# Optimization experiments

Measured on AMD Instinct MI355X. Metric: run time of the kernel, lower is better.

The kernel has to match this reference:

```python
import jax, jax.numpy as jnp
import numpy as np

CLS_COST, BBOX_COST, GIOU_COST = 2.0, 5.0, 2.0


def box_cxcywh_to_xyxy(b):
    cx, cy, w, h = b[..., 0], b[..., 1], b[..., 2], b[..., 3]
    return jnp.stack([cx - 0.5 * w, cy - 0.5 * h, cx + 0.5 * w, cy + 0.5 * h], axis=-1)


def generalized_box_iou(a, b):
    # a: [B,Q,4] xyxy, b: [B,T,4] xyxy -> [B,Q,T]
    area_a = (a[..., 2] - a[..., 0]) * (a[..., 3] - a[..., 1])  # [B,Q]
    area_b = (b[..., 2] - b[..., 0]) * (b[..., 3] - b[..., 1])  # [B,T]
    lt = jnp.maximum(a[:, :, None, :2], b[:, None, :, :2])      # [B,Q,T,2]
    rb = jnp.minimum(a[:, :, None, 2:], b[:, None, :, 2:])
    wh = jnp.clip(rb - lt, 0.0)
    inter = wh[..., 0] * wh[..., 1]                              # [B,Q,T]
    union = area_a[:, :, None] + area_b[:, None, :] - inter
    iou = inter / union
    lt_c = jnp.minimum(a[:, :, None, :2], b[:, None, :, :2])
    rb_c = jnp.maximum(a[:, :, None, 2:], b[:, None, :, 2:])
    wh_c = jnp.clip(rb_c - lt_c, 0.0)
    area_c = wh_c[..., 0] * wh_c[..., 1]
    return iou - (area_c - union) / area_c


def setup_inputs() -> dict:
    key = jax.random.key(0)
    k1, k2, k3, k4 = jax.random.split(key, 4)
    B, Q, C, T = 256, 900, 80, 300
    pred_logits = jax.random.normal(k1, (B, Q, C), dtype=jnp.float32)
    pred_boxes = jax.random.uniform(k2, (B, Q, 4), dtype=jnp.float32)
    tgt_labels = jax.random.randint(k3, (B, T), 0, C)
    tgt_boxes = jax.random.uniform(k4, (B, T, 4), dtype=jnp.float32)
    return {"pred_logits": pred_logits, "pred_boxes": pred_boxes,
            "tgt_labels": tgt_labels, "tgt_boxes": tgt_boxes}


def reference(pred_logits, pred_boxes, tgt_labels, tgt_boxes):
    # cost_class[b,q,t] = -sigmoid(logits)[b,q,labels[b,t]]
    prob = jax.nn.sigmoid(pred_logits)                              # [B,Q,C]
    cost_class = -jnp.take_along_axis(prob, tgt_labels[:, None, :], axis=2)  # [B,Q,T]
    # L1 cdist in cxcywh space
    cost_bbox = jnp.abs(pred_boxes[:, :, None, :] - tgt_boxes[:, None, :, :]).sum(-1)
    cost_giou = -generalized_box_iou(box_cxcywh_to_xyxy(pred_boxes),
                                     box_cxcywh_to_xyxy(tgt_boxes))
    return CLS_COST * cost_class + BBOX_COST * cost_bbox + GIOU_COST * cost_giou
```

## Files before the change

### kernel.cpp

```cpp
#include <hip/hip_runtime.h>

#define QDIM 900
#define CDIM 80
#define TDIM 300
#define QPB 36
#define QPW 9
#define NQB (QDIM / QPB)

typedef float floatx4 __attribute__((ext_vector_type(4)));

struct TgtReg {
    float x0, y0, x1, y1;
    float cx, cy, w, h;
    float area;
    int   lab;
};

__device__ __forceinline__ float cost_one(
    float ax0, float ay0, float ax1, float ay1,
    float acx, float acy, float aw, float ah, float area_a,
    const float* __restrict__ clsrow, const TgtReg& t)
{
    float clsv = clsrow[t.lab];

    float M0x = fmaxf(ax0, t.x0);
    float m1x = fminf(ax1, t.x1);
    float iwr = m1x - M0x;
    float iw  = fmaxf(iwr, 0.0f);
    float cw  = (aw + t.w) - iwr;

    float M0y = fmaxf(ay0, t.y0);
    float m1y = fminf(ay1, t.y1);
    float ihr = m1y - M0y;
    float ih  = fmaxf(ihr, 0.0f);
    float ch  = (ah + t.h) - ihr;

    float inter = iw * ih;
    float areac = cw * ch;
    float uni   = (area_a + t.area) - inter;

    float num   = fmaf(uni, uni, inter * areac);
    float den   = uni * areac;
    float ratio = num * __builtin_amdgcn_rcpf(den);

    float l1 = fabsf(acx - t.cx) + fabsf(acy - t.cy)
             + fabsf(aw - t.w)   + fabsf(ah - t.h);

    float acc = fmaf(5.0f, l1, clsv);
    return fmaf(-2.0f, ratio, acc);
}

__device__ __forceinline__ TgtReg load_tgt(const float4* tb4, const int* lb, int t)
{
    TgtReg r;
    float4 v = tb4[t];
    r.cx = v.x; r.cy = v.y; r.w = v.z; r.h = v.w;
    float hw = 0.5f * v.z, hh = 0.5f * v.w;
    r.x0 = v.x - hw; r.y0 = v.y - hh;
    r.x1 = v.x + hw; r.y1 = v.y + hh;
    r.area = v.z * v.w;
    r.lab = lb[t];
    return r;
}

__global__ __launch_bounds__(256, 4) void matcher_cost_kernel(
    const float* __restrict__ pred_logits,
    const float* __restrict__ pred_boxes,
    const int*   __restrict__ tgt_labels,
    const float* __restrict__ tgt_boxes,
    float* __restrict__ out)
{
    __shared__ float s_cls[QPB * CDIM];

    const int tid = threadIdx.x;
    const int b  = blockIdx.x / NQB;
    const int q0 = (blockIdx.x % NQB) * QPB;

    const float* lg = pred_logits + ((size_t)b * QDIM + q0) * CDIM;
    for (int i = tid; i < QPB * CDIM; i += 256) {
        float x = lg[i];
        s_cls[i] = 2.0f * __builtin_amdgcn_rcpf(1.0f + __expf(x));
    }
    __syncthreads();

    const int wave = tid >> 6;
    const int lane = tid & 63;

    const float4* tb4 = reinterpret_cast<const float4*>(tgt_boxes) + (size_t)b * TDIM;
    const int*    lb  = tgt_labels + (size_t)b * TDIM;

    TgtReg A[4];
    #pragma unroll
    for (int i = 0; i < 4; ++i) A[i] = load_tgt(tb4, lb, 4 * lane + i);

    const bool bok = lane < (TDIM - 256);
    const int  tB  = bok ? (256 + lane) : (TDIM - 1);
    TgtReg Bt = load_tgt(tb4, lb, tB);

    const int qw = q0 + wave * QPW;
    const float4* pb4 = reinterpret_cast<const float4*>(pred_boxes) + (size_t)b * QDIM + qw;
    float* orow0 = out + ((size_t)b * QDIM + qw) * TDIM;

    #pragma unroll 1
    for (int j = 0; j < QPW; ++j) {
        float4 a = pb4[j];
        const float hw = 0.5f * a.z, hh = 0.5f * a.w;
        const float ax0 = a.x - hw, ay0 = a.y - hh;
        const float ax1 = a.x + hw, ay1 = a.y + hh;
        const float area_a = a.z * a.w;
        const float* clsrow = s_cls + (wave * QPW + j) * CDIM;
        float* po = orow0 + j * TDIM;

        floatx4 res;
        res.x = cost_one(ax0, ay0, ax1, ay1, a.x, a.y, a.z, a.w, area_a, clsrow, A[0]);
        res.y = cost_one(ax0, ay0, ax1, ay1, a.x, a.y, a.z, a.w, area_a, clsrow, A[1]);
        res.z = cost_one(ax0, ay0, ax1, ay1, a.x, a.y, a.z, a.w, area_a, clsrow, A[2]);
        res.w = cost_one(ax0, ay0, ax1, ay1, a.x, a.y, a.z, a.w, area_a, clsrow, A[3]);
        __builtin_nontemporal_store(res, reinterpret_cast<floatx4*>(po) + lane);

        float cB = cost_one(ax0, ay0, ax1, ay1, a.x, a.y, a.z, a.w, area_a, clsrow, Bt);
        if (bok)
            __builtin_nontemporal_store(cB, po + 256 + lane);
    }
}

extern "C" void kernel_launch(void* const* d_in, const int* in_sizes, int n_in,
                              void* d_out, int out_size, void* d_ws, size_t ws_size,
                              hipStream_t stream) {
    const float* pred_logits = (const float*)d_in[0];
    const float* pred_boxes  = (const float*)d_in[1];
    const int*   tgt_labels  = (const int*)d_in[2];
    const float* tgt_boxes   = (const float*)d_in[3];
    float* out = (float*)d_out;

    const int B = in_sizes[0] / (QDIM * CDIM);
    dim3 grid(B * NQB);
    dim3 block(256);
    matcher_cost_kernel<<<grid, block, 0, stream>>>(pred_logits, pred_boxes,
                                                    tgt_labels, tgt_boxes, out);
}
```

Measured before the change: 86.99 us.

## Shrink per-target register state, recompute width/area and raise occupancy hint

Each thread now keeps only the xyxy corners and the label for its five targets, instead of ten values per target. Width, height, area and the L1 distance are recomputed from the corners in every cost evaluation. Launch bounds go from 4 to 7 waves per SIMD, and the next prediction box is prefetched one iteration ahead. The goal is lower VGPR use and higher occupancy so memory latency is better hidden, at the cost of extra ALU work per output.

```diff
diff --git a/kernel.cpp b/kernel.cpp
--- a/kernel.cpp
+++ b/kernel.cpp
@@ -9,61 +9,47 @@
 
 typedef float floatx4 __attribute__((ext_vector_type(4)));
 
-struct TgtReg {
-    float x0, y0, x1, y1;
-    float cx, cy, w, h;
-    float area;
-    int   lab;
-};
-
 __device__ __forceinline__ float cost_one(
     float ax0, float ay0, float ax1, float ay1,
-    float acx, float acy, float aw, float ah, float area_a,
-    const float* __restrict__ clsrow, const TgtReg& t)
+    float aw, float ah, float area_a,
+    const float* __restrict__ cls_j,
+    float bx0, float by0, float bx1, float by1, int lab)
 {
-    float clsv = clsrow[t.lab];
+    float clsv = cls_j[lab];
 
-    float M0x = fmaxf(ax0, t.x0);
-    float m1x = fminf(ax1, t.x1);
+    float M0x = fmaxf(ax0, bx0);
+    float m1x = fminf(ax1, bx1);
     float iwr = m1x - M0x;
     float iw  = fmaxf(iwr, 0.0f);
-    float cw  = (aw + t.w) - iwr;
-
-    float M0y = fmaxf(ay0, t.y0);
-    float m1y = fminf(ay1, t.y1);
+    float bw  = bx1 - bx0;
+    float cw  = (aw + bw) - iwr;
+    float M0y = fmaxf(ay0, by0);
+    float m1y = fminf(ay1, by1);
     float ihr = m1y - M0y;
     float ih  = fmaxf(ihr, 0.0f);
-    float ch  = (ah + t.h) - ihr;
+    float bh  = by1 - by0;
+    float ch  = (ah + bh) - ihr;
 
-    float inter = iw * ih;
-    float areac = cw * ch;
-    float uni   = (area_a + t.area) - inter;
+    float inter  = iw * ih;
+    float areac  = cw * ch;
+    float area_b = bw * bh;
+    float uni    = (area_a + area_b) - inter;
 
     float num   = fmaf(uni, uni, inter * areac);
     float den   = uni * areac;
     float ratio = num * __builtin_amdgcn_rcpf(den);
 
-    float l1 = fabsf(acx - t.cx) + fabsf(acy - t.cy)
-             + fabsf(aw - t.w)   + fabsf(ah - t.h);
+    float dx0 = ax0 - bx0, dx1 = ax1 - bx1;
+    float dy0 = ay0 - by0, dy1 = ay1 - by1;
+    float l1x = fmaf(0.5f, fabsf(dx0 + dx1), fabsf(dx1 - dx0));
+    float l1y = fmaf(0.5f, fabsf(dy0 + dy1), fabsf(dy1 - dy0));
+    float l1  = l1x + l1y;
 
     float acc = fmaf(5.0f, l1, clsv);
     return fmaf(-2.0f, ratio, acc);
 }
 
-__device__ __forceinline__ TgtReg load_tgt(const float4* tb4, const int* lb, int t)
-{
-    TgtReg r;
-    float4 v = tb4[t];
-    r.cx = v.x; r.cy = v.y; r.w = v.z; r.h = v.w;
-    float hw = 0.5f * v.z, hh = 0.5f * v.w;
-    r.x0 = v.x - hw; r.y0 = v.y - hh;
-    r.x1 = v.x + hw; r.y1 = v.y + hh;
-    r.area = v.z * v.w;
-    r.lab = lb[t];
-    return r;
-}
-
-__global__ __launch_bounds__(256, 4) void matcher_cost_kernel(
+__global__ __launch_bounds__(256, 7) void matcher_cost_kernel(
     const float* __restrict__ pred_logits,
     const float* __restrict__ pred_boxes,
     const int*   __restrict__ tgt_labels,
@@ -86,41 +72,57 @@
     const int wave = tid >> 6;
     const int lane = tid & 63;
 
-    const float4* tb4 = reinterpret_cast<const float4*>(tgt_boxes) + (size_t)b * TDIM;
-    const int*    lb  = tgt_labels + (size_t)b * TDIM;
-
-    TgtReg A[4];
-    #pragma unroll
-    for (int i = 0; i < 4; ++i) A[i] = load_tgt(tb4, lb, 4 * lane + i);
-
+    float tx0[5], ty0[5], tx1[5], ty1[5];
+    int   tlab[5];
+    {
+        const float4* tb4 = reinterpret_cast<const float4*>(tgt_boxes) + (size_t)b * TDIM;
+        const int*    lb  = tgt_labels + (size_t)b * TDIM;
+        #pragma unroll
+        for (int k = 0; k < 5; ++k) {
+            int t = (k < 4) ? (4 * lane + k) : (256 + lane);
+            if (t > TDIM - 1) t = TDIM - 1;
+            float4 v = tb4[t];
+            float hw = 0.5f * v.z, hh = 0.5f * v.w;
+            tx0[k] = v.x - hw; ty0[k] = v.y - hh;
+            tx1[k] = v.x + hw; ty1[k] = v.y + hh;
+            tlab[k] = lb[t];
+        }
+    }
     const bool bok = lane < (TDIM - 256);
-    const int  tB  = bok ? (256 + lane) : (TDIM - 1);
-    TgtReg Bt = load_tgt(tb4, lb, tB);
 
     const int qw = q0 + wave * QPW;
     const float4* pb4 = reinterpret_cast<const float4*>(pred_boxes) + (size_t)b * QDIM + qw;
     float* orow0 = out + ((size_t)b * QDIM + qw) * TDIM;
 
+    float4 a = pb4[0];
     #pragma unroll 1
     for (int j = 0; j < QPW; ++j) {
-        float4 a = pb4[j];
+        float4 an = pb4[(j < QPW - 1) ? (j + 1) : j];
         const float hw = 0.5f * a.z, hh = 0.5f * a.w;
         const float ax0 = a.x - hw, ay0 = a.y - hh;
         const float ax1 = a.x + hw, ay1 = a.y + hh;
+        const float aw = a.z, ah = a.w;
         const float area_a = a.z * a.w;
-        const float* clsrow = s_cls + (wave * QPW + j) * CDIM;
+        const float* cls_j = s_cls + (wave * QPW + j) * CDIM;
         float* po = orow0 + j * TDIM;
 
         floatx4 res;
-        res.x = cost_one(ax0, ay0, ax1, ay1, a.x, a.y, a.z, a.w, area_a, clsrow, A[0]);
-        res.y = cost_one(ax0, ay0, ax1, ay1, a.x, a.y, a.z, a.w, area_a, clsrow, A[1]);
-        res.z = cost_one(ax0, ay0, ax1, ay1, a.x, a.y, a.z, a.w, area_a, clsrow, A[2]);
-        res.w = cost_one(ax0, ay0, ax1, ay1, a.x, a.y, a.z, a.w, area_a, clsrow, A[3]);
+        res.x = cost_one(ax0, ay0, ax1, ay1, aw, ah, area_a, cls_j,
+                         tx0[0], ty0[0], tx1[0], ty1[0], tlab[0]);
+        res.y = cost_one(ax0, ay0, ax1, ay1, aw, ah, area_a, cls_j,
+                         tx0[1], ty0[1], tx1[1], ty1[1], tlab[1]);
+        res.z = cost_one(ax0, ay0, ax1, ay1, aw, ah, area_a, cls_j,
+                         tx0[2], ty0[2], tx1[2], ty1[2], tlab[2]);
+        res.w = cost_one(ax0, ay0, ax1, ay1, aw, ah, area_a, cls_j,
+                         tx0[3], ty0[3], tx1[3], ty1[3], tlab[3]);
         __builtin_nontemporal_store(res, reinterpret_cast<floatx4*>(po) + lane);
 
-        float cB = cost_one(ax0, ay0, ax1, ay1, a.x, a.y, a.z, a.w, area_a, clsrow, Bt);
+        float cB = cost_one(ax0, ay0, ax1, ay1, aw, ah, area_a, cls_j,
+                            tx0[4], ty0[4], tx1[4], ty1[4], tlab[4]);
         if (bok)
             __builtin_nontemporal_store(cB, po + 256 + lane);
+
+        a = an;
     }
 }
 
```

Result: slower. 95.86 us (+10.2%).
